# Kernel optimization log

Measured on AMD Instinct MI355X. Metric: run time of the kernel, lower is better.

## Reference

```python
import jax, jax.numpy as jnp
import numpy as np

IN_F = 4096
OUT_F = 4096
BATCH = 4096


def _dequantize(q, mn, mx):
    # Faithful to dequantize_to_float32: per-tensor affine using the *observed*
    # integer min/max of the stored tensor.
    q_min = q.min()
    q_max = q.max()
    scale = (mx - mn) / (q_max - q_min).astype(jnp.float32)
    return (q - q_min).astype(jnp.float32) * scale + mn


def setup_inputs() -> dict:
    key = jax.random.key(0)
    k1, k2, k3 = jax.random.split(key, 3)
    x = jax.random.normal(k1, (BATCH, IN_F), dtype=jnp.float32)
    # int8-valued weights/bias stored as int32 (same math; dequant uses tensor min/max)
    weight_q = jax.random.randint(k2, (OUT_F, IN_F), -128, 128, dtype=jnp.int32)
    bias_q = jax.random.randint(k3, (OUT_F,), -128, 128, dtype=jnp.int32)
    # per-tensor float range recorded at quantization time (original scales by 255 first,
    # so these ranges are on the scaled tensor; any floats work for correctness testing)
    weight_min = jnp.float32(-4.2)
    weight_max = jnp.float32(4.5)
    bias_min = jnp.float32(-1.3)
    bias_max = jnp.float32(1.1)
    return {
        "x": x,
        "weight_q": weight_q,
        "bias_q": bias_q,
        "weight_min": weight_min,
        "weight_max": weight_max,
        "bias_min": bias_min,
        "bias_max": bias_max,
    }


def reference(x, weight_q, bias_q, weight_min, weight_max, bias_min, bias_max):
    w = _dequantize(weight_q, weight_min, weight_max)   # [OUT_F, IN_F] fp32
    b = _dequantize(bias_q, bias_min, bias_max)         # [OUT_F] fp32
    # F.linear: x @ W^T + b
    return jnp.einsum("bi,oi->bo", x, w) + b
```

## Files before the change

kernel.cpp:

```cpp
#include <hip/hip_runtime.h>
#include <climits>

#define IN_F 4096
#define OUT_F 4096
#define BATCH 4096
#define NPART 1024

typedef __bf16 bf16x8 __attribute__((ext_vector_type(8)));
typedef float f32x4 __attribute__((ext_vector_type(4)));

__device__ __forceinline__ unsigned short f2bf_rne(float f) {
  unsigned int u = __float_as_uint(f);
  u += 0x7fffu + ((u >> 16) & 1u);
  return (unsigned short)(u >> 16);
}

__global__ __launch_bounds__(256) void k_convq(const int* __restrict__ q,
                                               unsigned short* __restrict__ qb,
                                               int* __restrict__ pmin,
                                               int* __restrict__ pmax) {
  const int n4 = (OUT_F * IN_F) / 4;
  const int stride = gridDim.x * blockDim.x;
  int vmin = INT_MAX, vmax = INT_MIN;
  const int4* q4 = (const int4*)q;
  ushort4* qb4 = (ushort4*)qb;
  for (int i = blockIdx.x * blockDim.x + threadIdx.x; i < n4; i += stride) {
    int4 v = q4[i];
    vmin = min(vmin, min(min(v.x, v.y), min(v.z, v.w)));
    vmax = max(vmax, max(max(v.x, v.y), max(v.z, v.w)));
    ushort4 h;
    h.x = f2bf_rne((float)v.x);
    h.y = f2bf_rne((float)v.y);
    h.z = f2bf_rne((float)v.z);
    h.w = f2bf_rne((float)v.w);
    qb4[i] = h;
  }
  for (int off = 32; off > 0; off >>= 1) {
    vmin = min(vmin, __shfl_down(vmin, off));
    vmax = max(vmax, __shfl_down(vmax, off));
  }
  __shared__ int rmin[4], rmax[4];
  const int wave = threadIdx.x >> 6;
  if ((threadIdx.x & 63) == 0) { rmin[wave] = vmin; rmax[wave] = vmax; }
  __syncthreads();
  if (threadIdx.x == 0) {
    pmin[blockIdx.x] = min(min(rmin[0], rmin[1]), min(rmin[2], rmin[3]));
    pmax[blockIdx.x] = max(max(rmax[0], rmax[1]), max(rmax[2], rmax[3]));
  }
}

__global__ __launch_bounds__(256) void k_wmm(const int* __restrict__ q,
                                             int* __restrict__ pmin,
                                             int* __restrict__ pmax) {
  const int n4 = (OUT_F * IN_F) / 4;
  const int stride = gridDim.x * blockDim.x;
  int vmin = INT_MAX, vmax = INT_MIN;
  const int4* q4 = (const int4*)q;
  for (int i = blockIdx.x * blockDim.x + threadIdx.x; i < n4; i += stride) {
    int4 v = q4[i];
    vmin = min(vmin, min(min(v.x, v.y), min(v.z, v.w)));
    vmax = max(vmax, max(max(v.x, v.y), max(v.z, v.w)));
  }
  for (int off = 32; off > 0; off >>= 1) {
    vmin = min(vmin, __shfl_down(vmin, off));
    vmax = max(vmax, __shfl_down(vmax, off));
  }
  __shared__ int rmin[4], rmax[4];
  const int wave = threadIdx.x >> 6;
  if ((threadIdx.x & 63) == 0) { rmin[wave] = vmin; rmax[wave] = vmax; }
  __syncthreads();
  if (threadIdx.x == 0) {
    pmin[blockIdx.x] = min(min(rmin[0], rmin[1]), min(rmin[2], rmin[3]));
    pmax[blockIdx.x] = max(max(rmax[0], rmax[1]), max(rmax[2], rmax[3]));
  }
}

__global__ __launch_bounds__(256) void k_convx(const float* __restrict__ x,
                                               unsigned short* __restrict__ xb,
                                               float* __restrict__ rowsum) {
  const int row = blockIdx.x;
  const float4* xr = (const float4*)(x + (size_t)row * IN_F);
  ushort4* xbr = (ushort4*)(xb + (size_t)row * IN_F);
  float s = 0.f;
  for (int i = threadIdx.x; i < IN_F / 4; i += blockDim.x) {
    float4 v = xr[i];
    s += (v.x + v.y) + (v.z + v.w);
    ushort4 h;
    h.x = f2bf_rne(v.x); h.y = f2bf_rne(v.y);
    h.z = f2bf_rne(v.z); h.w = f2bf_rne(v.w);
    xbr[i] = h;
  }
  __shared__ float red[4];
  for (int off = 32; off > 0; off >>= 1) s += __shfl_down(s, off);
  if ((threadIdx.x & 63) == 0) red[threadIdx.x >> 6] = s;
  __syncthreads();
  if (threadIdx.x == 0) rowsum[row] = (red[0] + red[1]) + (red[2] + red[3]);
}

__global__ __launch_bounds__(256) void k_scal(const int* __restrict__ pmin,
                                              const int* __restrict__ pmax, int npart,
                                              const int* __restrict__ bq,
                                              const float* __restrict__ wmn,
                                              const float* __restrict__ wmx,
                                              const float* __restrict__ bmn,
                                              const float* __restrict__ bmx,
                                              float* __restrict__ scal) {
  int vmin = INT_MAX, vmax = INT_MIN;
  for (int i = threadIdx.x; i < npart; i += 256) {
    vmin = min(vmin, pmin[i]);
    vmax = max(vmax, pmax[i]);
  }
  int bmin = INT_MAX, bmaxv = INT_MIN;
  for (int i = threadIdx.x; i < OUT_F; i += 256) {
    int v = bq[i];
    bmin = min(bmin, v);
    bmaxv = max(bmaxv, v);
  }
  for (int off = 32; off > 0; off >>= 1) {
    vmin = min(vmin, __shfl_down(vmin, off));
    vmax = max(vmax, __shfl_down(vmax, off));
    bmin = min(bmin, __shfl_down(bmin, off));
    bmaxv = max(bmaxv, __shfl_down(bmaxv, off));
  }
  __shared__ int r[4][4];
  const int wave = threadIdx.x >> 6;
  if ((threadIdx.x & 63) == 0) {
    r[wave][0] = vmin; r[wave][1] = vmax; r[wave][2] = bmin; r[wave][3] = bmaxv;
  }
  __syncthreads();
  if (threadIdx.x == 0) {
    int qmin = min(min(r[0][0], r[1][0]), min(r[2][0], r[3][0]));
    int qmax = max(max(r[0][1], r[1][1]), max(r[2][1], r[3][1]));
    int qbmin = min(min(r[0][2], r[1][2]), min(r[2][2], r[3][2]));
    int qbmax = max(max(r[0][3], r[1][3]), max(r[2][3], r[3][3]));
    float ws = (*wmx - *wmn) / (float)(qmax - qmin);
    scal[0] = ws;
    scal[1] = *wmn - ws * (float)qmin;
    float bs = (*bmx - *bmn) / (float)(qbmax - qbmin);
    scal[2] = bs;
    scal[3] = *bmn - bs * (float)qbmin;
  }
}

__device__ __forceinline__ void load_lds16(const unsigned short* g, unsigned short* l) {
  __builtin_amdgcn_global_load_lds(
      (const __attribute__((address_space(1))) unsigned int*)g,
      (__attribute__((address_space(3))) unsigned int*)l, 16, 0, 0);
}

__global__ __launch_bounds__(256) void k_gemm(
    const unsigned short* __restrict__ A,
    const unsigned short* __restrict__ B,
    const int* __restrict__ bq,
    const float* __restrict__ rowsum,
    const float* __restrict__ scal,
    float* __restrict__ C) {
  __shared__ unsigned short As[128 * 32];
  __shared__ unsigned short Bs[128 * 32];

  const int tid = threadIdx.x;
  const int wave = tid >> 6;
  const int lane = tid & 63;
  const int bm = blockIdx.x * 128;
  const int bn = blockIdx.y * 128;

  const int wm = (wave & 1) * 64;
  const int wn = (wave >> 1) * 64;
  const int row16 = lane & 15;
  const int quad = lane >> 4;

  const int c0 = wave * 2;
  const int r0 = c0 * 16 + (lane >> 2);
  const int r1 = r0 + 16;
  const int ccol = (lane & 3) * 8;
  const unsigned short* Ap0 = A + (size_t)(bm + r0) * IN_F + ccol;
  const unsigned short* Ap1 = A + (size_t)(bm + r1) * IN_F + ccol;
  const unsigned short* Bp0 = B + (size_t)(bn + r0) * IN_F + ccol;
  const unsigned short* Bp1 = B + (size_t)(bn + r1) * IN_F + ccol;
  unsigned short* As0 = &As[c0 * 512];
  unsigned short* As1 = &As[(c0 + 1) * 512];
  unsigned short* Bs0 = &Bs[c0 * 512];
  unsigned short* Bs1 = &Bs[(c0 + 1) * 512];

  f32x4 acc[4][4] = {};

  for (int k0 = 0; k0 < IN_F; k0 += 32) {
    load_lds16(Ap0 + k0, As0);
    load_lds16(Ap1 + k0, As1);
    load_lds16(Bp0 + k0, Bs0);
    load_lds16(Bp1 + k0, Bs1);
    __syncthreads();

    bf16x8 af[4], bfr[4];
#pragma unroll
    for (int i = 0; i < 4; ++i)
      af[i] = *(const bf16x8*)&As[(wm + i * 16 + row16) * 32 + quad * 8];
#pragma unroll
    for (int i = 0; i < 4; ++i)
      bfr[i] = *(const bf16x8*)&Bs[(wn + i * 16 + row16) * 32 + quad * 8];
#pragma unroll
    for (int mi = 0; mi < 4; ++mi)
#pragma unroll
      for (int ni = 0; ni < 4; ++ni)
        acc[mi][ni] = __builtin_amdgcn_mfma_f32_16x16x32_bf16(af[mi], bfr[ni], acc[mi][ni], 0, 0, 0);

    __syncthreads();
  }

  const float wsc = scal[0], wbe = scal[1], bsc = scal[2], bbe = scal[3];
#pragma unroll
  for (int ni = 0; ni < 4; ++ni) {
    const int gn = bn + wn + ni * 16 + row16;
    const float bdq = bsc * (float)bq[gn] + bbe;
#pragma unroll
    for (int mi = 0; mi < 4; ++mi) {
      const int gm0 = bm + wm + mi * 16 + quad * 4;
#pragma unroll
      for (int r = 0; r < 4; ++r) {
        const int gm = gm0 + r;
        C[(size_t)gm * OUT_F + gn] = wsc * acc[mi][ni][r] + wbe * rowsum[gm] + bdq;
      }
    }
  }
}

__global__ void k_naive(const float* __restrict__ x, const int* __restrict__ wq,
                        const int* __restrict__ bq, const float* __restrict__ scal,
                        float* __restrict__ out) {
  const int o = blockIdx.x * blockDim.x + threadIdx.x;
  const int b = blockIdx.y;
  const float* xr = x + (size_t)b * IN_F;
  const int* wr = wq + (size_t)o * IN_F;
  float s = 0.f, sx = 0.f;
  for (int k = 0; k < IN_F; ++k) {
    float xv = xr[k];
    s += xv * (float)wr[k];
    sx += xv;
  }
  out[(size_t)b * OUT_F + o] =
      scal[0] * s + scal[1] * sx + scal[2] * (float)bq[o] + scal[3];
}

extern "C" void kernel_launch(void* const* d_in, const int* in_sizes, int n_in,
                              void* d_out, int out_size, void* d_ws, size_t ws_size,
                              hipStream_t stream) {
  const float* x = (const float*)d_in[0];
  const int* wq = (const int*)d_in[1];
  const int* bq = (const int*)d_in[2];
  const float* wmn = (const float*)d_in[3];
  const float* wmx = (const float*)d_in[4];
  const float* bmn = (const float*)d_in[5];
  const float* bmx = (const float*)d_in[6];
  float* out = (float*)d_out;

  char* ws = (char*)d_ws;
  float* scal = (float*)ws;
  int* pmin = (int*)(ws + 64);
  int* pmax = (int*)(ws + 64 + NPART * 4);
  float* rowsum = (float*)(ws + 64 + 2 * NPART * 4);
  unsigned short* xb = (unsigned short*)(ws + 32768);
  unsigned short* qb = xb + (size_t)BATCH * IN_F;
  const size_t needed = 32768 + (size_t)BATCH * IN_F * 2 + (size_t)OUT_F * IN_F * 2;

  if (ws_size >= needed) {
    k_convq<<<NPART, 256, 0, stream>>>(wq, qb, pmin, pmax);
    k_convx<<<BATCH, 256, 0, stream>>>(x, xb, rowsum);
    k_scal<<<1, 256, 0, stream>>>(pmin, pmax, NPART, bq, wmn, wmx, bmn, bmx, scal);
    dim3 grid(BATCH / 128, OUT_F / 128);
    k_gemm<<<grid, 256, 0, stream>>>(xb, qb, bq, rowsum, scal, out);
  } else {
    k_wmm<<<NPART, 256, 0, stream>>>(wq, pmin, pmax);
    k_scal<<<1, 256, 0, stream>>>(pmin, pmax, NPART, bq, wmn, wmx, bmn, bmx, scal);
    k_naive<<<dim3(OUT_F / 256, BATCH), 256, 0, stream>>>(x, wq, bq, scal, out);
  }
}
```

Measured before the change: 360.4 us.

## Fuse weight and activation conversion kernels and XOR-swizzle GEMM LDS layout

Merges the weight int-to-bf16 conversion with min/max reduction and the activation fp32-to-bf16 conversion with row sums into one launch. Blocks beyond NPART handle four rows each, one row per wave, so no shared-memory reduction is needed. Separately, the GEMM applies an XOR swizzle to the column chunk used when loading global data into LDS, and the same swizzle on reads, to cut LDS bank conflicts on the fragment loads. The swizzle must line up with the load_lds16 write pattern, otherwise the results are wrong.

New measurement: 357.8 us. Within noise of the previous version (-0.7%).

```diff
diff --git a/kernel.cpp b/kernel.cpp
--- a/kernel.cpp
+++ b/kernel.cpp
@@ -15,37 +15,61 @@
   return (unsigned short)(u >> 16);
 }
 
-__global__ __launch_bounds__(256) void k_convq(const int* __restrict__ q,
-                                               unsigned short* __restrict__ qb,
-                                               int* __restrict__ pmin,
-                                               int* __restrict__ pmax) {
-  const int n4 = (OUT_F * IN_F) / 4;
-  const int stride = gridDim.x * blockDim.x;
-  int vmin = INT_MAX, vmax = INT_MIN;
-  const int4* q4 = (const int4*)q;
-  ushort4* qb4 = (ushort4*)qb;
-  for (int i = blockIdx.x * blockDim.x + threadIdx.x; i < n4; i += stride) {
-    int4 v = q4[i];
-    vmin = min(vmin, min(min(v.x, v.y), min(v.z, v.w)));
-    vmax = max(vmax, max(max(v.x, v.y), max(v.z, v.w)));
-    ushort4 h;
-    h.x = f2bf_rne((float)v.x);
-    h.y = f2bf_rne((float)v.y);
-    h.z = f2bf_rne((float)v.z);
-    h.w = f2bf_rne((float)v.w);
-    qb4[i] = h;
-  }
-  for (int off = 32; off > 0; off >>= 1) {
-    vmin = min(vmin, __shfl_down(vmin, off));
-    vmax = max(vmax, __shfl_down(vmax, off));
-  }
-  __shared__ int rmin[4], rmax[4];
-  const int wave = threadIdx.x >> 6;
-  if ((threadIdx.x & 63) == 0) { rmin[wave] = vmin; rmax[wave] = vmax; }
-  __syncthreads();
-  if (threadIdx.x == 0) {
-    pmin[blockIdx.x] = min(min(rmin[0], rmin[1]), min(rmin[2], rmin[3]));
-    pmax[blockIdx.x] = max(max(rmax[0], rmax[1]), max(rmax[2], rmax[3]));
+__global__ __launch_bounds__(256) void k_conv(const float* __restrict__ x,
+                                              const int* __restrict__ q,
+                                              unsigned short* __restrict__ xb,
+                                              unsigned short* __restrict__ qb,
+                                              float* __restrict__ rowsum,
+                                              int* __restrict__ pmin,
+                                              int* __restrict__ pmax) {
+  if (blockIdx.x < NPART) {
+    const int n4 = (OUT_F * IN_F) / 4;
+    const int stride = NPART * 256;
+    int vmin = INT_MAX, vmax = INT_MIN;
+    const int4* q4 = (const int4*)q;
+    ushort4* qb4 = (ushort4*)qb;
+    for (int i = blockIdx.x * 256 + threadIdx.x; i < n4; i += stride) {
+      int4 v = q4[i];
+      vmin = min(vmin, min(min(v.x, v.y), min(v.z, v.w)));
+      vmax = max(vmax, max(max(v.x, v.y), max(v.z, v.w)));
+      ushort4 h;
+      h.x = f2bf_rne((float)v.x);
+      h.y = f2bf_rne((float)v.y);
+      h.z = f2bf_rne((float)v.z);
+      h.w = f2bf_rne((float)v.w);
+      qb4[i] = h;
+    }
+    for (int off = 32; off > 0; off >>= 1) {
+      vmin = min(vmin, __shfl_down(vmin, off));
+      vmax = max(vmax, __shfl_down(vmax, off));
+    }
+    __shared__ int rmin[4], rmax[4];
+    const int wave = threadIdx.x >> 6;
+    if ((threadIdx.x & 63) == 0) { rmin[wave] = vmin; rmax[wave] = vmax; }
+    __syncthreads();
+    if (threadIdx.x == 0) {
+      pmin[blockIdx.x] = min(min(rmin[0], rmin[1]), min(rmin[2], rmin[3]));
+      pmax[blockIdx.x] = max(max(rmax[0], rmax[1]), max(rmax[2], rmax[3]));
+    }
+  } else {
+    const int wave = threadIdx.x >> 6;
+    const int lane = threadIdx.x & 63;
+    const int row = (blockIdx.x - NPART) * 4 + wave;
+    const float4* xr = (const float4*)(x + (size_t)row * IN_F);
+    ushort4* xbr = (ushort4*)(xb + (size_t)row * IN_F);
+    float s = 0.f;
+#pragma unroll
+    for (int it = 0; it < IN_F / 4 / 64; ++it) {
+      const int i = it * 64 + lane;
+      float4 v = xr[i];
+      s += (v.x + v.y) + (v.z + v.w);
+      ushort4 h;
+      h.x = f2bf_rne(v.x); h.y = f2bf_rne(v.y);
+      h.z = f2bf_rne(v.z); h.w = f2bf_rne(v.w);
+      xbr[i] = h;
+    }
+    for (int off = 32; off > 0; off >>= 1) s += __shfl_down(s, off);
+    if (lane == 0) rowsum[row] = s;
   }
 }
 
@@ -73,28 +97,6 @@
     pmin[blockIdx.x] = min(min(rmin[0], rmin[1]), min(rmin[2], rmin[3]));
     pmax[blockIdx.x] = max(max(rmax[0], rmax[1]), max(rmax[2], rmax[3]));
   }
-}
-
-__global__ __launch_bounds__(256) void k_convx(const float* __restrict__ x,
-                                               unsigned short* __restrict__ xb,
-                                               float* __restrict__ rowsum) {
-  const int row = blockIdx.x;
-  const float4* xr = (const float4*)(x + (size_t)row * IN_F);
-  ushort4* xbr = (ushort4*)(xb + (size_t)row * IN_F);
-  float s = 0.f;
-  for (int i = threadIdx.x; i < IN_F / 4; i += blockDim.x) {
-    float4 v = xr[i];
-    s += (v.x + v.y) + (v.z + v.w);
-    ushort4 h;
-    h.x = f2bf_rne(v.x); h.y = f2bf_rne(v.y);
-    h.z = f2bf_rne(v.z); h.w = f2bf_rne(v.w);
-    xbr[i] = h;
-  }
-  __shared__ float red[4];
-  for (int off = 32; off > 0; off >>= 1) s += __shfl_down(s, off);
-  if ((threadIdx.x & 63) == 0) red[threadIdx.x >> 6] = s;
-  __syncthreads();
-  if (threadIdx.x == 0) rowsum[row] = (red[0] + red[1]) + (red[2] + red[3]);
 }
 
 __global__ __launch_bounds__(256) void k_scal(const int* __restrict__ pmin,
@@ -172,7 +174,7 @@
   const int c0 = wave * 2;
   const int r0 = c0 * 16 + (lane >> 2);
   const int r1 = r0 + 16;
-  const int ccol = (lane & 3) * 8;
+  const int ccol = ((lane & 3) ^ ((lane >> 3) & 3)) * 8;
   const unsigned short* Ap0 = A + (size_t)(bm + r0) * IN_F + ccol;
   const unsigned short* Ap1 = A + (size_t)(bm + r1) * IN_F + ccol;
   const unsigned short* Bp0 = B + (size_t)(bn + r0) * IN_F + ccol;
@@ -182,6 +184,8 @@
   unsigned short* Bs0 = &Bs[c0 * 512];
   unsigned short* Bs1 = &Bs[(c0 + 1) * 512];
 
+  const int cread = (quad ^ ((lane >> 1) & 3)) * 8;
+
   f32x4 acc[4][4] = {};
 
   for (int k0 = 0; k0 < IN_F; k0 += 32) {
@@ -194,10 +198,10 @@
     bf16x8 af[4], bfr[4];
 #pragma unroll
     for (int i = 0; i < 4; ++i)
-      af[i] = *(const bf16x8*)&As[(wm + i * 16 + row16) * 32 + quad * 8];
+      af[i] = *(const bf16x8*)&As[(wm + i * 16 + row16) * 32 + cread];
 #pragma unroll
     for (int i = 0; i < 4; ++i)
-      bfr[i] = *(const bf16x8*)&Bs[(wn + i * 16 + row16) * 32 + quad * 8];
+      bfr[i] = *(const bf16x8*)&Bs[(wn + i * 16 + row16) * 32 + cread];
 #pragma unroll
     for (int mi = 0; mi < 4; ++mi)
 #pragma unroll
@@ -263,8 +267,7 @@
   const size_t needed = 32768 + (size_t)BATCH * IN_F * 2 + (size_t)OUT_F * IN_F * 2;
 
   if (ws_size >= needed) {
-    k_convq<<<NPART, 256, 0, stream>>>(wq, qb, pmin, pmax);
-    k_convx<<<BATCH, 256, 0, stream>>>(x, xb, rowsum);
+    k_conv<<<2 * NPART, 256, 0, stream>>>(x, wq, xb, qb, rowsum, pmin, pmax);
     k_scal<<<1, 256, 0, stream>>>(pmin, pmax, NPART, bq, wmn, wmx, bmn, bmx, scal);
     dim3 grid(BATCH / 128, OUT_F / 128);
     k_gemm<<<grid, 256, 0, stream>>>(xb, qb, bq, rowsum, scal, out);
```
